# Performance work log

Hardware: AMD Instinct MI355X
Metric: run time of the kernel (lower is better)

Reference implementation:

```python
import jax, jax.numpy as jnp
from jax import lax
import numpy as np

D_MODEL = 512
D_PROJ = 256
PATCH = 4
NL = 8
D_STATE = 16
D_CONV = 4
EXPAND = 2
D_INNER = EXPAND * D_MODEL          # 1024
DT_RANK = (D_MODEL + 15) // 16      # 32
B = 4
SEQ = 1024
NF = 1
EPS = 1e-5


def setup_inputs() -> dict:
    key = jax.random.key(0)
    ks = jax.random.split(key, 12)
    s = 0.02
    def rn(k, shape):
        return jax.random.normal(k, shape, jnp.float32) * s
    A_init = jnp.log(jnp.arange(1, D_STATE + 1, dtype=jnp.float32))  # (n,)
    return {
        "time_series": jax.random.normal(ks[0], (B, SEQ, NF), jnp.float32),
        "mask": jnp.ones((B, SEQ), jnp.int32),
        "emb_w": rn(ks[1], (D_MODEL, PATCH)),
        "emb_b": jnp.zeros((D_MODEL,), jnp.float32),
        "norm_w": jnp.ones((NL, D_MODEL), jnp.float32),
        "in_w": rn(ks[2], (NL, 2, 2 * D_INNER, D_MODEL)),
        "conv_w": rn(ks[3], (NL, 2, D_INNER, D_CONV)),
        "conv_b": jnp.zeros((NL, 2, D_INNER), jnp.float32),
        "xproj_w": rn(ks[4], (NL, 2, DT_RANK + 2 * D_STATE, D_INNER)),
        "dt_w": rn(ks[5], (NL, 2, D_INNER, DT_RANK)),
        "dt_b": jnp.full((NL, 2, D_INNER), float(np.log(np.expm1(0.01))), jnp.float32),
        "A_log": jnp.broadcast_to(A_init, (NL, 2, D_INNER, D_STATE)) + jnp.zeros((NL, 2, D_INNER, D_STATE), jnp.float32),
        "Dp": jnp.ones((NL, 2, D_INNER), jnp.float32),
        "out_w": rn(ks[6], (NL, 2, D_MODEL, D_INNER)),
        "proj_w": rn(ks[7], (PATCH * D_PROJ, D_MODEL)),
        "proj_b": jnp.zeros((PATCH * D_PROJ,), jnp.float32),
    }


def rmsnorm(x, w):
    return x * lax.rsqrt(jnp.mean(x * x, axis=-1, keepdims=True) + EPS) * w


def mamba(x, in_w, conv_w, conv_b, xproj_w, dt_w, dt_b, A_log, Dp, out_w):
    # x: (B, L, D_MODEL)
    Bsz, L, _ = x.shape
    xz = jnp.einsum('bld,ed->ble', x, in_w)                 # (B,L,2*d_inner)
    u, z = jnp.split(xz, 2, axis=-1)                         # each (B,L,d_inner)
    # depthwise causal conv1d along L
    u_t = jnp.transpose(u, (0, 2, 1))                        # (B,d_inner,L)
    u_pad = jnp.pad(u_t, ((0, 0), (0, 0), (D_CONV - 1, 0)))
    conv = lax.conv_general_dilated(
        u_pad, conv_w[:, None, :], window_strides=(1,), padding='VALID',
        feature_group_count=D_INNER, dimension_numbers=('NCH', 'OIH', 'NCH'))
    u = jax.nn.silu(jnp.transpose(conv + conv_b[None, :, None], (0, 2, 1)))  # (B,L,d_inner)
    x_dbl = jnp.einsum('ble,re->blr', u, xproj_w)            # (B,L,dt_rank+2n)
    dt, Bm, C = jnp.split(x_dbl, [DT_RANK, DT_RANK + D_STATE], axis=-1)
    delta = jax.nn.softplus(jnp.einsum('blr,er->ble', dt, dt_w) + dt_b)  # (B,L,d_inner)
    A = -jnp.exp(A_log)                                      # (d_inner,n)

    def step(h, inp):
        d_t, B_t, C_t, u_t = inp                             # (B,e),(B,n),(B,n),(B,e)
        dA = jnp.exp(d_t[..., None] * A)                     # (B,e,n)
        h = dA * h + (d_t * u_t)[..., None] * B_t[:, None, :]
        y = jnp.einsum('ben,bn->be', h, C_t)
        return h, y

    h0 = jnp.zeros((Bsz, D_INNER, D_STATE), x.dtype)
    xs = (jnp.moveaxis(delta, 1, 0), jnp.moveaxis(Bm, 1, 0),
          jnp.moveaxis(C, 1, 0), jnp.moveaxis(u, 1, 0))
    _, ys = lax.scan(step, h0, xs)                           # ys: (L,B,e)
    y = jnp.moveaxis(ys, 0, 1) + u * Dp
    y = y * jax.nn.silu(z)
    return jnp.einsum('ble,de->bld', y, out_w)               # (B,L,D_MODEL)


def reference(time_series, mask, emb_w, emb_b, norm_w, in_w, conv_w, conv_b,
              xproj_w, dt_w, dt_b, A_log, Dp, out_w, proj_w, proj_b):
    Bsz, S, F_ = time_series.shape
    NP = S // PATCH  # S is a multiple of PATCH
    patches = time_series.reshape(Bsz, NP, PATCH, F_)
    patches = jnp.transpose(patches, (0, 3, 1, 2)).reshape(Bsz, F_ * NP, PATCH)
    x = patches @ emb_w.T + emb_b                            # (B, F*NP, D_MODEL)
    for i in range(NL):
        res = x
        xn = rmsnorm(x, norm_w[i])
        yf = mamba(xn, in_w[i, 0], conv_w[i, 0], conv_b[i, 0], xproj_w[i, 0],
                   dt_w[i, 0], dt_b[i, 0], A_log[i, 0], Dp[i, 0], out_w[i, 0])
        yb = mamba(jnp.flip(xn, axis=1), in_w[i, 1], conv_w[i, 1], conv_b[i, 1],
                   xproj_w[i, 1], dt_w[i, 1], dt_b[i, 1], A_log[i, 1], Dp[i, 1], out_w[i, 1])
        x = yf + jnp.flip(yb, axis=1) + res
    proj = x @ proj_w.T + proj_b                             # (B, F*NP, PATCH*D_PROJ)
    le = proj.reshape(Bsz, F_, NP, PATCH, D_PROJ)
    le = jnp.transpose(le, (0, 2, 3, 1, 4)).reshape(Bsz, NP * PATCH, F_, D_PROJ)
    return le[:, :S]
```

## Files before the change

### kernel.cpp

```cpp
#include <hip/hip_runtime.h>
#include <hip/hip_bf16.h>

#define DM 512
#define DI 1024
#define DSTATE 16
#define DTR 32
#define NLAYER 8
#define BS 4
#define LL 256
#define MT 1024
#define DPROJ 256
#define CL 32
#define NCH (LL/CL)

typedef unsigned short u16;
typedef __attribute__((ext_vector_type(8))) short short8;
typedef __attribute__((ext_vector_type(8))) unsigned short ushort8v;
typedef __attribute__((ext_vector_type(4))) float f32x4;

__device__ __forceinline__ float sigmoidf_(float x){ return 1.f/(1.f+__expf(-x)); }

__device__ __forceinline__ u16 f2bf(float f){
  unsigned u = __float_as_uint(f);
  u = (u + 0x7FFF + ((u>>16)&1)) >> 16;
  return (u16)u;
}

template<int CTRL>
__device__ __forceinline__ float dpp_ror_add(float x){
  int y = __builtin_amdgcn_update_dpp(0, __float_as_int(x), CTRL, 0xF, 0xF, false);
  return x + __int_as_float(y);
}
__device__ __forceinline__ float sum16_dpp(float x){
  x = dpp_ror_add<0x128>(x);
  x = dpp_ror_add<0x124>(x);
  x = dpp_ror_add<0x122>(x);
  x = dpp_ror_add<0x121>(x);
  return x;
}

__global__ __launch_bounds__(256) void embed_k(const float* __restrict__ ts,
    const float* __restrict__ ew, const float* __restrict__ eb, float* __restrict__ x){
  int idx = blockIdx.x*256 + threadIdx.x;
  int m = idx >> 9, d = idx & 511;
  int b = m >> 8, np_ = m & 255;
  const float* t0 = ts + b*1024 + np_*4;
  float acc = eb[d];
  #pragma unroll
  for (int p=0;p<4;p++) acc = fmaf(t0[p], ew[d*4+p], acc);
  x[idx] = acc;
}

__global__ __launch_bounds__(256) void wcastall_k(
    const float* __restrict__ w_in, const float* __restrict__ w_out,
    const float* __restrict__ w_xp, const float* __restrict__ w_dt,
    const float* __restrict__ w_pj, u16* __restrict__ dst){
  long t = (long)blockIdx.x*256 + threadIdx.x;
  long e16 = t*16;
  const float* src; long o;
  if      (e16 < 16777216) { src = w_in;  o = e16; }
  else if (e16 < 25165824) { src = w_out; o = e16 - 16777216; }
  else if (e16 < 26214400) { src = w_xp;  o = e16 - 25165824; }
  else if (e16 < 26738688) { src = w_dt;  o = e16 - 26214400; }
  else                     { src = w_pj;  o = e16 - 26738688; }
  float4 a = *(const float4*)(src + o);
  float4 b = *(const float4*)(src + o + 4);
  float4 c = *(const float4*)(src + o + 8);
  float4 d = *(const float4*)(src + o + 12);
  ushort8v r0, r1;
  r0[0]=f2bf(a.x); r0[1]=f2bf(a.y); r0[2]=f2bf(a.z); r0[3]=f2bf(a.w);
  r0[4]=f2bf(b.x); r0[5]=f2bf(b.y); r0[6]=f2bf(b.z); r0[7]=f2bf(b.w);
  r1[0]=f2bf(c.x); r1[1]=f2bf(c.y); r1[2]=f2bf(c.z); r1[3]=f2bf(c.w);
  r1[4]=f2bf(d.x); r1[5]=f2bf(d.y); r1[6]=f2bf(d.z); r1[7]=f2bf(d.w);
  *(ushort8v*)(dst + e16) = r0;
  *(ushort8v*)(dst + e16 + 8) = r1;
}

__global__ __launch_bounds__(256) void rmscomb_k(float* __restrict__ x,
    const float* __restrict__ yout,
    const float* __restrict__ nw, u16* __restrict__ xnbf, u16* __restrict__ xnfbf){
  int m = blockIdx.x, t = threadIdx.x;
  int b = m>>8, l = m&255, mf = (b<<8)+(255-l);
  float2 v = *(const float2*)&x[(long)m*DM + t*2];
  if (yout){
    float2 f = *(const float2*)&yout[(long)m*DM + t*2];
    float2 g = *(const float2*)&yout[(long)MT*DM + (long)mf*DM + t*2];
    v.x += f.x + g.x; v.y += f.y + g.y;
    *(float2*)&x[(long)m*DM + t*2] = v;
  }
  float ss = v.x*v.x + v.y*v.y;
  ss += __shfl_down(ss,32); ss += __shfl_down(ss,16); ss += __shfl_down(ss,8);
  ss += __shfl_down(ss,4);  ss += __shfl_down(ss,2);  ss += __shfl_down(ss,1);
  __shared__ float ps[4];
  if ((t&63)==0) ps[t>>6] = ss;
  __syncthreads();
  float tot = ps[0]+ps[1]+ps[2]+ps[3];
  float rs = rsqrtf(tot*(1.f/DM) + 1e-5f);
  ushort2 o; o.x = f2bf(v.x*rs*nw[t*2]); o.y = f2bf(v.y*rs*nw[t*2+1]);
  *(ushort2*)&xnbf [(long)m *DM + t*2] = o;
  *(ushort2*)&xnfbf[(long)mf*DM + t*2] = o;
}

__global__ __launch_bounds__(256) void combcast_k(const float* __restrict__ x,
    const float* __restrict__ yout, u16* __restrict__ xbf){
  int idx = blockIdx.x*256 + threadIdx.x;
  int m = idx >> 7, c4 = idx & 127;
  int b = m>>8, l = m&255, mf = (b<<8)+(255-l);
  float4 r = ((const float4*)x)[idx];
  float4 f = ((const float4*)yout)[idx];
  float4 g = ((const float4*)(yout + (long)MT*DM))[(long)mf*128 + c4];
  ushort4 o;
  o.x = f2bf(r.x + f.x + g.x); o.y = f2bf(r.y + f.y + g.y);
  o.z = f2bf(r.z + f.z + g.z); o.w = f2bf(r.w + f.w + g.w);
  ((ushort4*)xbf)[idx] = o;
}

template<int BM,int BN,int SPLITK,int EPI>
__global__ __launch_bounds__(256) void mfma_nt(
    const u16* __restrict__ A, int lda, long sA,
    const u16* __restrict__ W, int ldw, long sW,
    const float* __restrict__ bias, long sBias,
    float* __restrict__ C, int ldc, long sC,
    int M, int N, int K)
{
  constexpr int WM = BM/2, WN = BN/2;
  constexpr int MI = WM/16, NI = WN/16;
  int z = blockIdx.z;
  int dir = z / SPLITK, kc = z % SPLITK;
  int Klen = K / SPLITK;
  int kbase = kc * Klen;
  A += (long)dir * sA;
  W += (long)dir * sW;
  if (SPLITK > 1) C += (long)z * M * N; else C += (long)dir * sC;
  if (EPI==1) bias += (long)dir * sBias;

  __shared__ u16 Al[BM*32];
  __shared__ u16 Wl[BN*32];
  int tid = threadIdx.x;
  int lane = tid & 63;
  int wave = tid >> 6;
  int wm0 = (wave>>1)*WM, wn0 = (wave&1)*WN;
  int m0 = blockIdx.y*BM, n0 = blockIdx.x*BN;
  int l16 = lane>>4, l15 = lane&15;

  f32x4 acc[MI][NI] = {};

  for (int k0=0; k0<Klen; k0+=32){
    #pragma unroll
    for (int it=0; it<BM*4/256; ++it){
      int ch = it*256 + tid;
      int row = ch % BM, kk = ch / BM;
      const u16* g = A + (long)(m0+row)*lda + kbase + k0 + kk*8;
      __builtin_amdgcn_global_load_lds(
          (const __attribute__((address_space(1))) void*)g,
          (__attribute__((address_space(3))) void*)(Al + ch*8), 16, 0, 0);
    }
    #pragma unroll
    for (int it=0; it<BN*4/256; ++it){
      int ch = it*256 + tid;
      int row = ch % BN, kk = ch / BN;
      const u16* g = W + (long)(n0+row)*ldw + kbase + k0 + kk*8;
      __builtin_amdgcn_global_load_lds(
          (const __attribute__((address_space(1))) void*)g,
          (__attribute__((address_space(3))) void*)(Wl + ch*8), 16, 0, 0);
    }
    __syncthreads();
    short8 a[MI], b[NI];
    #pragma unroll
    for (int i=0;i<MI;i++)
      a[i] = *(const short8*)&Al[(l16*BM + wm0 + i*16 + l15)*8];
    #pragma unroll
    for (int j=0;j<NI;j++)
      b[j] = *(const short8*)&Wl[(l16*BN + wn0 + j*16 + l15)*8];
    #pragma unroll
    for (int i=0;i<MI;i++)
      #pragma unroll
      for (int j=0;j<NI;j++)
        acc[i][j] = __builtin_amdgcn_mfma_f32_16x16x32_bf16(a[i], b[j], acc[i][j], 0,0,0);
    __syncthreads();
  }
  #pragma unroll
  for (int i=0;i<MI;i++){
    #pragma unroll
    for (int j=0;j<NI;j++){
      #pragma unroll
      for (int r=0;r<4;r++){
        int m = m0 + wm0 + i*16 + l16*4 + r;
        int n = n0 + wn0 + j*16 + l15;
        float v = acc[i][j][r];
        if (EPI==1){
          v += bias[n];
          v = (v>20.f) ? v : log1pf(__expf(v));
          C[(long)m*ldc + n] = v;
        } else if (EPI==2){
          v += bias[n];
          int bb = m>>8, np_ = m&255, p = n>>8, dp = n&255;
          C[((long)(bb*1024 + np_*4 + p))*256 + dp] = v;
        } else {
          C[(long)m*ldc + n] = v;
        }
      }
    }
  }
}

__global__ __launch_bounds__(256) void xreduce_k(const float* __restrict__ part,
    float* __restrict__ xdbl, u16* __restrict__ dtbf){
  int idx = blockIdx.x*256 + threadIdx.x;
  int d = idx >> 16, off = idx & 65535;
  float s = 0.f;
  #pragma unroll
  for (int kc=0; kc<8; ++kc) s += part[((d*8+kc)<<16) + off];
  xdbl[idx] = s;
  int col = off & 63;
  if (col < 32){
    int m = off >> 6;
    dtbf[((long)d*MT + m)*32 + col] = f2bf(s);
  }
}

__global__ __launch_bounds__(256) void conv_silu_k(const float* __restrict__ xz,
    const float* __restrict__ cw, const float* __restrict__ cb,
    float* __restrict__ u, u16* __restrict__ ubf){
  int idx = blockIdx.x*256 + threadIdx.x;
  int e = idx & (DI-1);
  int grp = idx >> 10;
  int dir = grp >> 8;
  int b   = (grp >> 6) & 3;
  int l0  = (grp & 63) * 4;
  long dm0 = (long)dir*MT + b*LL + l0;
  const float* w = cw + ((long)dir*DI + e)*4;
  float w0=w[0], w1=w[1], w2=w[2], w3=w[3];
  float bias = cb[dir*DI + e];
  const float* src = xz + dm0*2048 + e;
  float vb[7];
  #pragma unroll
  for (int j=0;j<7;j++){
    int l = l0 - 3 + j;
    vb[j] = (l >= 0) ? src[(long)(j-3)*2048] : 0.f;
  }
  #pragma unroll
  for (int j=0;j<4;j++){
    float acc = bias;
    acc = fmaf(w0, vb[j],   acc);
    acc = fmaf(w1, vb[j+1], acc);
    acc = fmaf(w2, vb[j+2], acc);
    acc = fmaf(w3, vb[j+3], acc);
    float v = acc * sigmoidf_(acc);
    u  [(dm0+j)*DI + e] = v;
    ubf[(dm0+j)*DI + e] = f2bf(v);
  }
}

__global__ __launch_bounds__(256) void scan_k(
    const float* __restrict__ delta, const float* __restrict__ u,
    const float* __restrict__ xz, const float* __restrict__ xdbl,
    const float* __restrict__ A_log, const float* __restrict__ Dp,
    u16* __restrict__ ygbf)
{
  int t = threadIdx.x;
  int n = t & 15, el = t >> 4;
  int ec = blockIdx.x, b = blockIdx.y, dir = blockIdx.z;
  int e0 = ec*16;
  int e = e0 + el;
  float Av = -__expf(A_log[((long)dir*DI + e)*16 + n]);
  float Dv = Dp[dir*DI + e];
  long mbase = (long)dir*MT + b*LL;
  const float* dp_ = delta + mbase*DI;
  const float* up_ = u     + mbase*DI;
  const float* zp_ = xz    + mbase*2048 + 1024;
  const float* bc_ = xdbl  + mbase*64 + 32;
  u16* yp_ = ygbf + mbase*DI;

  __shared__ float sDU[2][CL][32];
  __shared__ float sBC[2][CL][32];
  __shared__ float sy[CL][16];

  int lb  = t >> 3,        jb = (t & 7) * 4;
  int tt  = t & 127;
  int ld_ = tt >> 2,       ed = (tt & 3) * 4;

  float4 pbc, pdu;
  auto load_pre = [&](int c){
    long l0 = (long)c*CL;
    pbc = *(const float4*)&bc_[(l0+lb)*64 + jb];
    pdu = (t < 128) ? *(const float4*)&dp_[(l0+ld_)*DI + e0 + ed]
                    : *(const float4*)&up_[(l0+ld_)*DI + e0 + ed];
  };
  auto write_pre = [&](int buf){
    *(float4*)&sBC[buf][lb][jb] = pbc;
    if (t < 128) *(float4*)&sDU[buf][ld_][ed]      = pdu;
    else         *(float4*)&sDU[buf][ld_][16+ed]   = pdu;
  };

  load_pre(0);
  write_pre(0);
  load_pre(1);
  __syncthreads();

  float h = 0.f;
  for (int c = 0; c < NCH; ++c){
    int cur = c & 1;
    float4 zc;
    if (t < 128) zc = *(const float4*)&zp_[((long)c*CL + ld_)*2048 + e0 + ed];

    const float* du = &sDU[cur][0][el];
    const float* bc = &sBC[cur][0][n];
    #pragma unroll
    for (int c8 = 0; c8 < 4; ++c8){
      const float* du8 = du + c8*256;
      const float* bc8 = bc + c8*256;
      #pragma unroll
      for (int l8 = 0; l8 < 8; ++l8){
        float dv = du8[l8*32],  uv = du8[l8*32 + 16];
        float Bv = bc8[l8*32],  Cv = bc8[l8*32 + 16];
        float dA = __expf(dv*Av);
        h = fmaf(dA, h, dv*uv*Bv);
        float yc = sum16_dpp(h*Cv);
        if (n==0) sy[c8*8+l8][el] = yc + uv*Dv;
      }
    }
    __syncthreads();
    if (c+1 < NCH){
      write_pre(cur^1);
      if (c+2 < NCH) load_pre(c+2);
    }
    if (t < 128){
      float4 y4 = *(const float4*)&sy[ld_][ed];
      float gx = zc.x*sigmoidf_(zc.x), gy = zc.y*sigmoidf_(zc.y);
      float gz = zc.z*sigmoidf_(zc.z), gw = zc.w*sigmoidf_(zc.w);
      ushort4 o; o.x=f2bf(y4.x*gx); o.y=f2bf(y4.y*gy); o.z=f2bf(y4.z*gz); o.w=f2bf(y4.w*gw);
      *(ushort4*)&yp_[((long)c*CL + ld_)*DI + e0 + ed] = o;
    }
    __syncthreads();
  }
}

extern "C" void kernel_launch(void* const* d_in, const int* in_sizes, int n_in,
                              void* d_out, int out_size, void* d_ws, size_t ws_size,
                              hipStream_t stream){
  const float* ts   = (const float*)d_in[0];
  const float* ew   = (const float*)d_in[2];
  const float* eb   = (const float*)d_in[3];
  const float* nw   = (const float*)d_in[4];
  const float* inw  = (const float*)d_in[5];
  const float* cw   = (const float*)d_in[6];
  const float* cb   = (const float*)d_in[7];
  const float* xpw  = (const float*)d_in[8];
  const float* dtw  = (const float*)d_in[9];
  const float* dtb  = (const float*)d_in[10];
  const float* alog = (const float*)d_in[11];
  const float* dpp  = (const float*)d_in[12];
  const float* outw = (const float*)d_in[13];
  const float* pw   = (const float*)d_in[14];
  const float* pb   = (const float*)d_in[15];
  float* out = (float*)d_out;

  float* ws   = (float*)d_ws;
  float* x    = ws;
  float* xz   = ws + 524288;
  float* u    = ws + 4718592;
  float* xdbl = ws + 6815744;
  float* delta= ws + 6946816;
  float* yout = ws + 9043968;
  float* xpart= ws + 10092544;
  u16* ub     = (u16*)(ws + 11141120);
  u16* xn_bf  = ub;
  u16* u_bf   = ub + 1048576;
  u16* yg_bf  = ub + 3145728;
  u16* x_bf   = ub + 5242880;
  u16* dt_bf  = ub + 5767168;
  u16* wb     = ub + 5832704;
  u16* wb_in  = wb;
  u16* wb_out = wb + 16777216;
  u16* wb_xp  = wb + 25165824;
  u16* wb_dt  = wb + 26214400;
  u16* wb_pj  = wb + 26738688;

  dim3 blk(256);

  embed_k<<<MT*DM/256, blk, 0, stream>>>(ts, ew, eb, x);
  wcastall_k<<<6656, blk, 0, stream>>>(inw, outw, xpw, dtw, pw, wb);

  for (int i=0;i<NLAYER;i++){
    rmscomb_k<<<MT, blk, 0, stream>>>(x, i ? yout : nullptr, nw + i*DM,
        xn_bf, xn_bf + MT*DM);
    mfma_nt<64,128,1,0><<<dim3(16,16,2), blk, 0, stream>>>(
        xn_bf, DM, (long)MT*DM, wb_in + (long)i*2097152, DM, 1048576,
        nullptr, 0, xz, 2048, (long)MT*2048, MT, 2048, DM);
    conv_silu_k<<<2048, blk, 0, stream>>>(xz, cw + (long)i*2*DI*4, cb + i*2*DI, u, u_bf);
    mfma_nt<64,64,8,0><<<dim3(1,16,16), blk, 0, stream>>>(
        u_bf, DI, (long)MT*DI, wb_xp + (long)i*131072, DI, 65536,
        nullptr, 0, xpart, 64, 0, MT, 64, DI);
    xreduce_k<<<512, blk, 0, stream>>>(xpart, xdbl, dt_bf);
    mfma_nt<128,64,1,1><<<dim3(16,8,2), blk, 0, stream>>>(
        dt_bf, DTR, (long)MT*DTR, wb_dt + (long)i*65536, DTR, 32768,
        dtb + (long)i*2*DI, DI, delta, DI, (long)MT*DI, MT, DI, DTR);
    scan_k<<<dim3(64, BS, 2), blk, 0, stream>>>(delta, u, xz, xdbl,
        alog + (long)i*2*DI*16, dpp + i*2*DI, yg_bf);
    mfma_nt<64,64,1,0><<<dim3(8,16,2), blk, 0, stream>>>(
        yg_bf, DI, (long)MT*DI, wb_out + (long)i*1048576, DI, 524288,
        nullptr, 0, yout, DM, (long)MT*DM, MT, DM, DI);
  }
  combcast_k<<<MT*DM/4/256, blk, 0, stream>>>(x, yout, x_bf);
  mfma_nt<64,64,1,2><<<dim3(16,16,1), blk, 0, stream>>>(
      x_bf, DM, 0, wb_pj, DM, 0, pb, 0, out, 1024, 0, MT, 1024, DM);
}
```

Baseline: 839.6 us.

## Fuse dt projection and softplus into scan kernel, drop fp32 u buffer

```diff
diff --git a/kernel.cpp b/kernel.cpp
--- a/kernel.cpp
+++ b/kernel.cpp
@@ -15,7 +15,6 @@
 
 typedef unsigned short u16;
 typedef __attribute__((ext_vector_type(8))) short short8;
-typedef __attribute__((ext_vector_type(8))) unsigned short ushort8v;
 typedef __attribute__((ext_vector_type(4))) float f32x4;
 
 __device__ __forceinline__ float sigmoidf_(float x){ return 1.f/(1.f+__expf(-x)); }
@@ -24,6 +23,9 @@
   unsigned u = __float_as_uint(f);
   u = (u + 0x7FFF + ((u>>16)&1)) >> 16;
   return (u16)u;
+}
+__device__ __forceinline__ float bf2f(u16 v){
+  return __uint_as_float(((unsigned)v) << 16);
 }
 
 template<int CTRL>
@@ -53,27 +55,18 @@
 
 __global__ __launch_bounds__(256) void wcastall_k(
     const float* __restrict__ w_in, const float* __restrict__ w_out,
-    const float* __restrict__ w_xp, const float* __restrict__ w_dt,
-    const float* __restrict__ w_pj, u16* __restrict__ dst){
-  long t = (long)blockIdx.x*256 + threadIdx.x;
-  long e16 = t*16;
+    const float* __restrict__ w_xp, const float* __restrict__ w_pj,
+    u16* __restrict__ dst){
+  int t = blockIdx.x*256 + threadIdx.x;
+  long e4 = (long)t*4;
   const float* src; long o;
-  if      (e16 < 16777216) { src = w_in;  o = e16; }
-  else if (e16 < 25165824) { src = w_out; o = e16 - 16777216; }
-  else if (e16 < 26214400) { src = w_xp;  o = e16 - 25165824; }
-  else if (e16 < 26738688) { src = w_dt;  o = e16 - 26214400; }
-  else                     { src = w_pj;  o = e16 - 26738688; }
-  float4 a = *(const float4*)(src + o);
-  float4 b = *(const float4*)(src + o + 4);
-  float4 c = *(const float4*)(src + o + 8);
-  float4 d = *(const float4*)(src + o + 12);
-  ushort8v r0, r1;
-  r0[0]=f2bf(a.x); r0[1]=f2bf(a.y); r0[2]=f2bf(a.z); r0[3]=f2bf(a.w);
-  r0[4]=f2bf(b.x); r0[5]=f2bf(b.y); r0[6]=f2bf(b.z); r0[7]=f2bf(b.w);
-  r1[0]=f2bf(c.x); r1[1]=f2bf(c.y); r1[2]=f2bf(c.z); r1[3]=f2bf(c.w);
-  r1[4]=f2bf(d.x); r1[5]=f2bf(d.y); r1[6]=f2bf(d.z); r1[7]=f2bf(d.w);
-  *(ushort8v*)(dst + e16) = r0;
-  *(ushort8v*)(dst + e16 + 8) = r1;
+  if      (e4 < 16777216) { src = w_in;  o = e4; }
+  else if (e4 < 25165824) { src = w_out; o = e4 - 16777216; }
+  else if (e4 < 26214400) { src = w_xp;  o = e4 - 25165824; }
+  else                    { src = w_pj;  o = e4 - 26214400; }
+  float4 v = *(const float4*)(src + o);
+  ushort4 r; r.x=f2bf(v.x); r.y=f2bf(v.y); r.z=f2bf(v.z); r.w=f2bf(v.w);
+  *(ushort4*)(dst + e4) = r;
 }
 
 __global__ __launch_bounds__(256) void rmscomb_k(float* __restrict__ x,
@@ -119,7 +112,7 @@
 __global__ __launch_bounds__(256) void mfma_nt(
     const u16* __restrict__ A, int lda, long sA,
     const u16* __restrict__ W, int ldw, long sW,
-    const float* __restrict__ bias, long sBias,
+    const float* __restrict__ bias,
     float* __restrict__ C, int ldc, long sC,
     int M, int N, int K)
 {
@@ -132,7 +125,6 @@
   A += (long)dir * sA;
   W += (long)dir * sW;
   if (SPLITK > 1) C += (long)z * M * N; else C += (long)dir * sC;
-  if (EPI==1) bias += (long)dir * sBias;
 
   __shared__ u16 Al[BM*32];
   __shared__ u16 Wl[BN*32];
@@ -188,11 +180,7 @@
         int m = m0 + wm0 + i*16 + l16*4 + r;
         int n = n0 + wn0 + j*16 + l15;
         float v = acc[i][j][r];
-        if (EPI==1){
-          v += bias[n];
-          v = (v>20.f) ? v : log1pf(__expf(v));
-          C[(long)m*ldc + n] = v;
-        } else if (EPI==2){
+        if (EPI==2){
           v += bias[n];
           int bb = m>>8, np_ = m&255, p = n>>8, dp = n&255;
           C[((long)(bb*1024 + np_*4 + p))*256 + dp] = v;
@@ -205,23 +193,18 @@
 }
 
 __global__ __launch_bounds__(256) void xreduce_k(const float* __restrict__ part,
-    float* __restrict__ xdbl, u16* __restrict__ dtbf){
+    float* __restrict__ xdbl){
   int idx = blockIdx.x*256 + threadIdx.x;
   int d = idx >> 16, off = idx & 65535;
   float s = 0.f;
   #pragma unroll
   for (int kc=0; kc<8; ++kc) s += part[((d*8+kc)<<16) + off];
   xdbl[idx] = s;
-  int col = off & 63;
-  if (col < 32){
-    int m = off >> 6;
-    dtbf[((long)d*MT + m)*32 + col] = f2bf(s);
-  }
 }
 
 __global__ __launch_bounds__(256) void conv_silu_k(const float* __restrict__ xz,
     const float* __restrict__ cw, const float* __restrict__ cb,
-    float* __restrict__ u, u16* __restrict__ ubf){
+    u16* __restrict__ ubf){
   int idx = blockIdx.x*256 + threadIdx.x;
   int e = idx & (DI-1);
   int grp = idx >> 10;
@@ -247,50 +230,67 @@
     acc = fmaf(w2, vb[j+2], acc);
     acc = fmaf(w3, vb[j+3], acc);
     float v = acc * sigmoidf_(acc);
-    u  [(dm0+j)*DI + e] = v;
     ubf[(dm0+j)*DI + e] = f2bf(v);
   }
 }
 
 __global__ __launch_bounds__(256) void scan_k(
-    const float* __restrict__ delta, const float* __restrict__ u,
-    const float* __restrict__ xz, const float* __restrict__ xdbl,
-    const float* __restrict__ A_log, const float* __restrict__ Dp,
-    u16* __restrict__ ygbf)
+    const u16* __restrict__ ubf, const float* __restrict__ xz,
+    const float* __restrict__ xdbl, const float* __restrict__ dtw,
+    const float* __restrict__ dtb, const float* __restrict__ A_log,
+    const float* __restrict__ Dp, u16* __restrict__ ygbf)
 {
   int t = threadIdx.x;
   int n = t & 15, el = t >> 4;
   int ec = blockIdx.x, b = blockIdx.y, dir = blockIdx.z;
-  int e0 = ec*16;
-  int e = e0 + el;
+  int e0 = ec*16, e = e0 + el;
   float Av = -__expf(A_log[((long)dir*DI + e)*16 + n]);
   float Dv = Dp[dir*DI + e];
   long mbase = (long)dir*MT + b*LL;
-  const float* dp_ = delta + mbase*DI;
-  const float* up_ = u     + mbase*DI;
-  const float* zp_ = xz    + mbase*2048 + 1024;
-  const float* bc_ = xdbl  + mbase*64 + 32;
+  const u16*  up_ = ubf + mbase*DI;
+  const float* zp_ = xz + mbase*2048 + 1024;
+  const float* xd_ = xdbl + mbase*64;
   u16* yp_ = ygbf + mbase*DI;
 
-  __shared__ float sDU[2][CL][32];
+  float wrow[32];
+  {
+    const float* wr = dtw + ((long)dir*DI + e0 + n)*32;
+    #pragma unroll
+    for (int r4=0;r4<8;r4++) *(float4*)&wrow[r4*4] = *(const float4*)&wr[r4*4];
+  }
+  float dtbv = dtb[dir*DI + e0 + n];
+
+  __shared__ float sdt[2][CL][32];
   __shared__ float sBC[2][CL][32];
-  __shared__ float sy[CL][16];
-
-  int lb  = t >> 3,        jb = (t & 7) * 4;
-  int tt  = t & 127;
-  int ld_ = tt >> 2,       ed = (tt & 3) * 4;
-
-  float4 pbc, pdu;
+  __shared__ float sU [2][CL][16];
+  __shared__ float sD [CL][16];
+  __shared__ float sy [CL][16];
+
+  float4 xv0, xv1; ushort4 uvv;
   auto load_pre = [&](int c){
     long l0 = (long)c*CL;
-    pbc = *(const float4*)&bc_[(l0+lb)*64 + jb];
-    pdu = (t < 128) ? *(const float4*)&dp_[(l0+ld_)*DI + e0 + ed]
-                    : *(const float4*)&up_[(l0+ld_)*DI + e0 + ed];
+    int f0 = t, f1 = t + 256;
+    xv0 = *(const float4*)&xd_[(l0 + (f0>>4))*64 + (f0&15)*4];
+    xv1 = *(const float4*)&xd_[(l0 + (f1>>4))*64 + (f1&15)*4];
+    if (t < 128) uvv = *(const ushort4*)&up_[(l0 + (t>>2))*DI + e0 + (t&3)*4];
   };
   auto write_pre = [&](int buf){
-    *(float4*)&sBC[buf][lb][jb] = pbc;
-    if (t < 128) *(float4*)&sDU[buf][ld_][ed]      = pdu;
-    else         *(float4*)&sDU[buf][ld_][16+ed]   = pdu;
+    {
+      int row = t>>4, c4 = (t&15)*4;
+      if (c4 < 32) *(float4*)&sdt[buf][row][c4] = xv0;
+      else         *(float4*)&sBC[buf][row][c4-32] = xv0;
+    }
+    {
+      int f1 = t + 256;
+      int row = f1>>4, c4 = (f1&15)*4;
+      if (c4 < 32) *(float4*)&sdt[buf][row][c4] = xv1;
+      else         *(float4*)&sBC[buf][row][c4-32] = xv1;
+    }
+    if (t < 128){
+      float4 uf;
+      uf.x = bf2f(uvv.x); uf.y = bf2f(uvv.y); uf.z = bf2f(uvv.z); uf.w = bf2f(uvv.w);
+      *(float4*)&sU[buf][t>>2][(t&3)*4] = uf;
+    }
   };
 
   load_pre(0);
@@ -301,19 +301,38 @@
   float h = 0.f;
   for (int c = 0; c < NCH; ++c){
     int cur = c & 1;
+    #pragma unroll
+    for (int j=0;j<2;j++){
+      int l = (t>>4)*2 + j;
+      float acc = dtbv;
+      #pragma unroll
+      for (int r4=0;r4<8;r4++){
+        float4 d4 = *(const float4*)&sdt[cur][l][r4*4];
+        acc = fmaf(d4.x, wrow[r4*4],   acc);
+        acc = fmaf(d4.y, wrow[r4*4+1], acc);
+        acc = fmaf(d4.z, wrow[r4*4+2], acc);
+        acc = fmaf(d4.w, wrow[r4*4+3], acc);
+      }
+      acc = (acc>20.f) ? acc : log1pf(__expf(acc));
+      sD[l][n] = acc;
+    }
     float4 zc;
-    if (t < 128) zc = *(const float4*)&zp_[((long)c*CL + ld_)*2048 + e0 + ed];
-
-    const float* du = &sDU[cur][0][el];
-    const float* bc = &sBC[cur][0][n];
+    if (t < 128) zc = *(const float4*)&zp_[((long)c*CL + (t>>2))*2048 + e0 + (t&3)*4];
+    __syncthreads();
+
+    const float* pD  = &sD[0][el];
+    const float* pU  = &sU[cur][0][el];
+    const float* pBC = &sBC[cur][0][n];
     #pragma unroll
     for (int c8 = 0; c8 < 4; ++c8){
-      const float* du8 = du + c8*256;
-      const float* bc8 = bc + c8*256;
+      const float* pD8  = pD  + c8*128;
+      const float* pU8  = pU  + c8*128;
+      const float* pBC8 = pBC + c8*256;
       #pragma unroll
       for (int l8 = 0; l8 < 8; ++l8){
-        float dv = du8[l8*32],  uv = du8[l8*32 + 16];
-        float Bv = bc8[l8*32],  Cv = bc8[l8*32 + 16];
+        float dv = pD8[l8*16];
+        float uv = pU8[l8*16];
+        float Bv = pBC8[l8*32], Cv = pBC8[l8*32 + 16];
         float dA = __expf(dv*Av);
         h = fmaf(dA, h, dv*uv*Bv);
         float yc = sum16_dpp(h*Cv);
@@ -326,11 +345,11 @@
       if (c+2 < NCH) load_pre(c+2);
     }
     if (t < 128){
-      float4 y4 = *(const float4*)&sy[ld_][ed];
+      float4 y4 = *(const float4*)&sy[t>>2][(t&3)*4];
       float gx = zc.x*sigmoidf_(zc.x), gy = zc.y*sigmoidf_(zc.y);
       float gz = zc.z*sigmoidf_(zc.z), gw = zc.w*sigmoidf_(zc.w);
       ushort4 o; o.x=f2bf(y4.x*gx); o.y=f2bf(y4.y*gy); o.z=f2bf(y4.z*gz); o.w=f2bf(y4.w*gw);
-      *(ushort4*)&yp_[((long)c*CL + ld_)*DI + e0 + ed] = o;
+      *(ushort4*)&yp_[((long)c*CL + (t>>2))*DI + e0 + (t&3)*4] = o;
     }
     __syncthreads();
   }
@@ -359,50 +378,44 @@
   float* ws   = (float*)d_ws;
   float* x    = ws;
   float* xz   = ws + 524288;
-  float* u    = ws + 4718592;
-  float* xdbl = ws + 6815744;
-  float* delta= ws + 6946816;
-  float* yout = ws + 9043968;
-  float* xpart= ws + 10092544;
-  u16* ub     = (u16*)(ws + 11141120);
+  float* xdbl = ws + 4718592;
+  float* yout = ws + 4849664;
+  float* xpart= ws + 5898240;
+  u16* ub     = (u16*)(ws + 6946816);
   u16* xn_bf  = ub;
   u16* u_bf   = ub + 1048576;
   u16* yg_bf  = ub + 3145728;
   u16* x_bf   = ub + 5242880;
-  u16* dt_bf  = ub + 5767168;
-  u16* wb     = ub + 5832704;
+  u16* wb     = ub + 5767168;
   u16* wb_in  = wb;
   u16* wb_out = wb + 16777216;
   u16* wb_xp  = wb + 25165824;
-  u16* wb_dt  = wb + 26214400;
-  u16* wb_pj  = wb + 26738688;
+  u16* wb_pj  = wb + 26214400;
 
   dim3 blk(256);
 
   embed_k<<<MT*DM/256, blk, 0, stream>>>(ts, ew, eb, x);
-  wcastall_k<<<6656, blk, 0, stream>>>(inw, outw, xpw, dtw, pw, wb);
+  wcastall_k<<<26112, blk, 0, stream>>>(inw, outw, xpw, pw, wb);
 
   for (int i=0;i<NLAYER;i++){
     rmscomb_k<<<MT, blk, 0, stream>>>(x, i ? yout : nullptr, nw + i*DM,
         xn_bf, xn_bf + MT*DM);
     mfma_nt<64,128,1,0><<<dim3(16,16,2), blk, 0, stream>>>(
         xn_bf, DM, (long)MT*DM, wb_in + (long)i*2097152, DM, 1048576,
-        nullptr, 0, xz, 2048, (long)MT*2048, MT, 2048, DM);
-    conv_silu_k<<<2048, blk, 0, stream>>>(xz, cw + (long)i*2*DI*4, cb + i*2*DI, u, u_bf);
+        nullptr, xz, 2048, (long)MT*2048, MT, 2048, DM);
+    conv_silu_k<<<2048, blk, 0, stream>>>(xz, cw + (long)i*2*DI*4, cb + i*2*DI, u_bf);
     mfma_nt<64,64,8,0><<<dim3(1,16,16), blk, 0, stream>>>(
         u_bf, DI, (long)MT*DI, wb_xp + (long)i*131072, DI, 65536,
-        nullptr, 0, xpart, 64, 0, MT, 64, DI);
-    xreduce_k<<<512, blk, 0, stream>>>(xpart, xdbl, dt_bf);
-    mfma_nt<128,64,1,1><<<dim3(16,8,2), blk, 0, stream>>>(
-        dt_bf, DTR, (long)MT*DTR, wb_dt + (long)i*65536, DTR, 32768,
-        dtb + (long)i*2*DI, DI, delta, DI, (long)MT*DI, MT, DI, DTR);
-    scan_k<<<dim3(64, BS, 2), blk, 0, stream>>>(delta, u, xz, xdbl,
+        nullptr, xpart, 64, 0, MT, 64, DI);
+    xreduce_k<<<512, blk, 0, stream>>>(xpart, xdbl);
+    scan_k<<<dim3(64, BS, 2), blk, 0, stream>>>(u_bf, xz, xdbl,
+        dtw + (long)i*2*DI*DTR, dtb + (long)i*2*DI,
         alog + (long)i*2*DI*16, dpp + i*2*DI, yg_bf);
     mfma_nt<64,64,1,0><<<dim3(8,16,2), blk, 0, stream>>>(
         yg_bf, DI, (long)MT*DI, wb_out + (long)i*1048576, DI, 524288,
-        nullptr, 0, yout, DM, (long)MT*DM, MT, DM, DI);
+        nullptr, yout, DM, (long)MT*DM, MT, DM, DI);
   }
   combcast_k<<<MT*DM/4/256, blk, 0, stream>>>(x, yout, x_bf);
   mfma_nt<64,64,1,2><<<dim3(16,16,1), blk, 0, stream>>>(
-      x_bf, DM, 0, wb_pj, DM, 0, pb, 0, out, 1024, 0, MT, 1024, DM);
-}
+      x_bf, DM, 0, wb_pj, DM, 0, pb, out, 1024, 0, MT, 1024, DM);
+}
```

Result: faster. 796.8 us (-5.1%).
